# Kernel tuning notes

Hardware: AMD Instinct MI355X
Metric: run time of the kernel (lower is better)

The kernel has to match this reference:

```python
import jax, jax.numpy as jnp
import numpy as np
import math

B, Q, CQ = 2, 2048, 512
H, D = 8, 64  # no_heads, c_hidden

def setup_inputs() -> dict:
    key = jax.random.key(0)
    ks = jax.random.split(key, 8)
    s = 0.02
    return {
        "q_x": jax.random.normal(ks[0], (B, Q, CQ), jnp.float32),
        "kv_x": jax.random.normal(ks[1], (B, Q, CQ), jnp.float32),
        "bias": jax.random.normal(ks[2], (B, 1, Q, Q), jnp.float32),
        "w_qkv": jax.random.normal(ks[3], (3 * H * D, CQ), jnp.float32) * s,
        "w_o": jax.random.normal(ks[4], (CQ, H * D), jnp.float32) * s,
        "b_o": jnp.zeros((CQ,), jnp.float32),
        "w_g": jax.random.normal(ks[5], (H * D, CQ), jnp.float32) * s,
        "b_g": jnp.zeros((H * D,), jnp.float32),
    }

def reference(q_x, kv_x, bias, w_qkv, w_o, b_o, w_g, b_g):
    # Fused QKV projection from q_x (kv_x is unused by the original module's _prep_qkv)
    qkv = jnp.einsum('bqc,ec->bqe', q_x, w_qkv)  # [B,Q,3*H*D]
    q, k, v = jnp.split(qkv, 3, axis=-1)
    q = q.reshape(B, Q, H, D) / math.sqrt(D)
    k = k.reshape(B, Q, H, D)
    v = v.reshape(B, Q, H, D)
    # scores + additive pairwise bias, softmax over keys
    scores = jnp.einsum('bqhd,bkhd->bhqk', q, k) + bias  # [B,H,Q,K]
    attn = jax.nn.softmax(scores, axis=-1)
    o = jnp.einsum('bhqk,bkhd->bqhd', attn, v)  # [B,Q,H,D]
    # sigmoid gating
    g = jax.nn.sigmoid(jnp.einsum('bqc,ec->bqe', q_x, w_g) + b_g).reshape(B, Q, H, D)
    o = o * g
    # output projection
    o = o.reshape(B, Q, H * D)
    return jnp.einsum('bqe,ce->bqc', o, w_o) + b_o
```

## Files before the change

kernel.cpp:

```cpp
#include <hip/hip_runtime.h>
#include <math.h>

#define B_  2
#define Q_  2048
#define CQ_ 512
#define H_  8
#define D_  64
#define M_  (B_*Q_)

typedef __bf16 bf16;
typedef __bf16 bf16x4 __attribute__((ext_vector_type(4)));
typedef __bf16 bf16x8 __attribute__((ext_vector_type(8)));
typedef float  f32x4  __attribute__((ext_vector_type(4)));

__device__ __forceinline__ void gl_lds16(const bf16* g, bf16* l) {
    __builtin_amdgcn_global_load_lds(
        (const __attribute__((address_space(1))) unsigned int*)g,
        (__attribute__((address_space(3))) unsigned int*)l, 16, 0, 0);
}

#define S0 (4096*512)
#define S1 (1536*512)
#define S2 (512*512)
#define S3 (512*512)
__global__ __launch_bounds__(256)
void convert_kernel(const float* __restrict__ qx, const float* __restrict__ wqkv,
                    const float* __restrict__ wg, const float* __restrict__ wo,
                    bf16* __restrict__ qxb, bf16* __restrict__ wcat, bf16* __restrict__ wob)
{
    const long long t = (long long)blockIdx.x * 256 + threadIdx.x;
    const long long e = t * 8;
    const float* src; bf16* dst;
    if (e < S0)                { src = qx + e;                  dst = qxb + e; }
    else if (e < S0 + S1)      { src = wqkv + (e - S0);         dst = wcat + (e - S0); }
    else if (e < S0 + S1 + S2) { src = wg + (e - S0 - S1);      dst = wcat + S1 + (e - S0 - S1); }
    else                       { src = wo + (e - S0 - S1 - S2); dst = wob + (e - S0 - S1 - S2); }
    const float4 a = *(const float4*)(src);
    const float4 b = *(const float4*)(src + 4);
    bf16x8 v;
    v[0] = (bf16)a.x; v[1] = (bf16)a.y; v[2] = (bf16)a.z; v[3] = (bf16)a.w;
    v[4] = (bf16)b.x; v[5] = (bf16)b.y; v[6] = (bf16)b.z; v[7] = (bf16)b.w;
    *(bf16x8*)dst = v;
}

template<int BM, int BN, int EPI>
__global__ __launch_bounds__(256)
void gemm_bf16(const bf16* __restrict__ A, const bf16* __restrict__ W,
               const float* __restrict__ bvec, float* __restrict__ fout,
               bf16* __restrict__ qb, bf16* __restrict__ kb, bf16* __restrict__ vb,
               bf16* __restrict__ gb)
{
    constexpr int MI = BM / 32, NJ = BN / 32;
    __shared__ __align__(16) bf16 As[BM * 32];
    __shared__ __align__(16) bf16 Bs[BN * 32];

    const int t = threadIdx.x;
    const int w = t >> 6, lane = t & 63;
    const int l15 = lane & 15, quad = lane >> 4;
    const int wm = w & 1, wn = w >> 1;
    const int bm = blockIdx.x * BM;
    const int bn = blockIdx.y * BN;

    f32x4 acc[MI][NJ] = {};

    const int rr = t >> 2;
    const int cc = (t & 3) * 8;

    for (int k0 = 0; k0 < 512; k0 += 32) {
        #pragma unroll
        for (int i = 0; i < BM / 64; ++i)
            gl_lds16(A + (size_t)(bm + i * 64 + rr) * 512 + k0 + cc,
                     As + (i * 64 + w * 16) * 32);
        #pragma unroll
        for (int i = 0; i < BN / 64; ++i)
            gl_lds16(W + (size_t)(bn + i * 64 + rr) * 512 + k0 + cc,
                     Bs + (i * 64 + w * 16) * 32);
        __asm__ volatile("s_waitcnt vmcnt(0)" ::: "memory");
        __syncthreads();

        bf16x8 af[MI], bfr[NJ];
        #pragma unroll
        for (int i = 0; i < MI; ++i)
            af[i] = *(const bf16x8*)(As + (wm * (BM / 2) + i * 16 + l15) * 32 + quad * 8);
        #pragma unroll
        for (int j = 0; j < NJ; ++j)
            bfr[j] = *(const bf16x8*)(Bs + (wn * (BN / 2) + j * 16 + l15) * 32 + quad * 8);
        #pragma unroll
        for (int i = 0; i < MI; ++i)
            #pragma unroll
            for (int j = 0; j < NJ; ++j)
                acc[i][j] = __builtin_amdgcn_mfma_f32_16x16x32_bf16(af[i], bfr[j], acc[i][j], 0, 0, 0);
        __syncthreads();
    }

    #pragma unroll
    for (int i = 0; i < MI; ++i) {
        #pragma unroll
        for (int r = 0; r < 4; ++r) {
            const int m = bm + wm * (BM / 2) + i * 16 + quad * 4 + r;
            const int b = m >> 11, qq = m & 2047;
            #pragma unroll
            for (int j = 0; j < NJ; ++j) {
                const int n = bn + wn * (BN / 2) + j * 16 + l15;
                const float c = acc[i][j][r];
                if constexpr (EPI == 0) {
                    const int part = n >> 9;
                    const int h = (n >> 6) & 7, d = n & 63;
                    if (part == 0)
                        qb[(((size_t)(b * H_ + h)) * Q_ + qq) * D_ + d] = (bf16)(c * 0.125f);
                    else if (part == 1)
                        kb[(((size_t)(b * H_ + h)) * Q_ + qq) * D_ + d] = (bf16)c;
                    else if (part == 2)
                        vb[(((size_t)(b * H_ + h)) * D_ + d) * Q_ + qq] = (bf16)c;
                    else {
                        const int gcol = n & 511;
                        const float x = c + bvec[gcol];
                        gb[(size_t)m * 512 + gcol] = (bf16)(1.f / (1.f + __expf(-x)));
                    }
                } else {
                    fout[(size_t)m * 512 + n] = c + bvec[n];
                }
            }
        }
    }
}

__global__ __launch_bounds__(256)
void attn_kernel(const bf16* __restrict__ qb, const bf16* __restrict__ kb,
                 const bf16* __restrict__ vb, const float* __restrict__ bias,
                 const bf16* __restrict__ g, bf16* __restrict__ og)
{
    __shared__ __align__(16) bf16 Ks[2][64 * 72];
    __shared__ __align__(16) bf16 Vs[2][64 * 72];
    __shared__ __align__(16) bf16 Ps[4][16 * 72];

    const int tid  = threadIdx.x;
    const int wv   = tid >> 6, lane = tid & 63;
    const int l15  = lane & 15, quad = lane >> 4;
    const int bh   = blockIdx.x;
    const int b    = bh >> 3, h = bh & 7;
    const int q0   = blockIdx.y * 64;
    const int qrow = q0 + wv * 16 + l15;

    const bf16* qptr = qb + ((size_t)bh * Q_ + qrow) * D_;
    const bf16x8 bq0 = *(const bf16x8*)(qptr + quad * 8);
    const bf16x8 bq1 = *(const bf16x8*)(qptr + 32 + quad * 8);

    f32x4 acc[4] = {};
    float m_run = -INFINITY, l_run = 0.f;

    const bf16*  kbase = kb + (size_t)bh * Q_ * D_;
    const bf16*  vbase = vb + (size_t)bh * D_ * Q_;
    const float* brow  = bias + ((size_t)b * Q_ + qrow) * Q_;

    const int sr  = tid >> 3;
    const int sc8 = (tid & 7) * 8;

    float4 kreg0, kreg1, vreg0, vreg1;
    float4 bias_cur[4], bias_nxt[4];

    kreg0 = *(const float4*)(kbase + (size_t)sr * 64 + sc8);
    kreg1 = *(const float4*)(kbase + (size_t)(32 + sr) * 64 + sc8);
    vreg0 = *(const float4*)(vbase + (size_t)sr * Q_ + sc8);
    vreg1 = *(const float4*)(vbase + (size_t)(32 + sr) * Q_ + sc8);
    #pragma unroll
    for (int kt = 0; kt < 4; ++kt)
        bias_cur[kt] = *(const float4*)(brow + kt * 16 + quad * 4);
    *(float4*)(Ks[0] + sr * 72 + sc8) = kreg0;
    *(float4*)(Ks[0] + (32 + sr) * 72 + sc8) = kreg1;
    *(float4*)(Vs[0] + sr * 72 + sc8) = vreg0;
    *(float4*)(Vs[0] + (32 + sr) * 72 + sc8) = vreg1;
    __syncthreads();

    int cur = 0;
    for (int t = 0; t < 32; ++t) {
        if (t < 31) {
            const int k0n = (t + 1) * 64;
            kreg0 = *(const float4*)(kbase + ((size_t)k0n + sr) * 64 + sc8);
            kreg1 = *(const float4*)(kbase + ((size_t)k0n + 32 + sr) * 64 + sc8);
            vreg0 = *(const float4*)(vbase + (size_t)sr * Q_ + k0n + sc8);
            vreg1 = *(const float4*)(vbase + (size_t)(32 + sr) * Q_ + k0n + sc8);
            #pragma unroll
            for (int kt = 0; kt < 4; ++kt)
                bias_nxt[kt] = *(const float4*)(brow + k0n + kt * 16 + quad * 4);
        }

        const bf16* Kc = Ks[cur];
        const bf16* Vc = Vs[cur];

        float sc[4][4];
        #pragma unroll
        for (int kt = 0; kt < 4; ++kt) {
            f32x4 sacc = {0.f, 0.f, 0.f, 0.f};
            const bf16* kp = Kc + (kt * 16 + l15) * 72 + quad * 8;
            const bf16x8 ak0 = *(const bf16x8*)(kp);
            const bf16x8 ak1 = *(const bf16x8*)(kp + 32);
            sacc = __builtin_amdgcn_mfma_f32_16x16x32_bf16(ak0, bq0, sacc, 0, 0, 0);
            sacc = __builtin_amdgcn_mfma_f32_16x16x32_bf16(ak1, bq1, sacc, 0, 0, 0);
            sc[kt][0] = sacc[0] + bias_cur[kt].x;
            sc[kt][1] = sacc[1] + bias_cur[kt].y;
            sc[kt][2] = sacc[2] + bias_cur[kt].z;
            sc[kt][3] = sacc[3] + bias_cur[kt].w;
        }

        float tmax = -INFINITY;
        #pragma unroll
        for (int kt = 0; kt < 4; ++kt)
            tmax = fmaxf(tmax, fmaxf(fmaxf(sc[kt][0], sc[kt][1]),
                                     fmaxf(sc[kt][2], sc[kt][3])));
        tmax = fmaxf(tmax, __shfl_xor(tmax, 16, 64));
        tmax = fmaxf(tmax, __shfl_xor(tmax, 32, 64));

        const float mn = fmaxf(m_run, tmax);
        const float alpha = __expf(m_run - mn);
        m_run = mn;

        float rsum = 0.f;
        #pragma unroll
        for (int kt = 0; kt < 4; ++kt)
            #pragma unroll
            for (int r = 0; r < 4; ++r) {
                sc[kt][r] = __expf(sc[kt][r] - mn);
                rsum += sc[kt][r];
            }
        rsum += __shfl_xor(rsum, 16, 64);
        rsum += __shfl_xor(rsum, 32, 64);
        l_run = l_run * alpha + rsum;
        #pragma unroll
        for (int dt = 0; dt < 4; ++dt) acc[dt] *= alpha;

        bf16* pw = Ps[wv] + l15 * 72;
        #pragma unroll
        for (int kt = 0; kt < 4; ++kt) {
            bf16x4 p4;
            p4[0] = (bf16)sc[kt][0]; p4[1] = (bf16)sc[kt][1];
            p4[2] = (bf16)sc[kt][2]; p4[3] = (bf16)sc[kt][3];
            *(bf16x4*)(pw + kt * 16 + quad * 4) = p4;
        }
        __asm__ volatile("s_waitcnt lgkmcnt(0)" ::: "memory");

        #pragma unroll
        for (int kt2 = 0; kt2 < 2; ++kt2) {
            const bf16x8 bp = *(const bf16x8*)(pw + kt2 * 32 + quad * 8);
            #pragma unroll
            for (int dt = 0; dt < 4; ++dt) {
                const bf16x8 av = *(const bf16x8*)(Vc + (dt * 16 + l15) * 72 + kt2 * 32 + quad * 8);
                acc[dt] = __builtin_amdgcn_mfma_f32_16x16x32_bf16(av, bp, acc[dt], 0, 0, 0);
            }
        }

        if (t < 31) {
            *(float4*)(Ks[cur ^ 1] + sr * 72 + sc8) = kreg0;
            *(float4*)(Ks[cur ^ 1] + (32 + sr) * 72 + sc8) = kreg1;
            *(float4*)(Vs[cur ^ 1] + sr * 72 + sc8) = vreg0;
            *(float4*)(Vs[cur ^ 1] + (32 + sr) * 72 + sc8) = vreg1;
            #pragma unroll
            for (int kt = 0; kt < 4; ++kt) bias_cur[kt] = bias_nxt[kt];
        }
        __syncthreads();
        cur ^= 1;
    }

    const float inv = 1.f / l_run;
    const size_t obase = ((size_t)(b * Q_ + qrow)) * 512 + h * 64;
    #pragma unroll
    for (int dt = 0; dt < 4; ++dt) {
        const bf16x4 gv = *(const bf16x4*)(g + obase + dt * 16 + quad * 4);
        bf16x4 ov;
        #pragma unroll
        for (int r = 0; r < 4; ++r)
            ov[r] = (bf16)(acc[dt][r] * inv * (float)gv[r]);
        *(bf16x4*)(og + obase + dt * 16 + quad * 4) = ov;
    }
}

extern "C" void kernel_launch(void* const* d_in, const int* in_sizes, int n_in,
                              void* d_out, int out_size, void* d_ws, size_t ws_size,
                              hipStream_t stream)
{
    const float* q_x   = (const float*)d_in[0];
    const float* bias  = (const float*)d_in[2];
    const float* w_qkv = (const float*)d_in[3];
    const float* w_o   = (const float*)d_in[4];
    const float* b_o   = (const float*)d_in[5];
    const float* w_g   = (const float*)d_in[6];
    const float* b_g   = (const float*)d_in[7];
    float* out = (float*)d_out;

    char* ws = (char*)d_ws;
    bf16* qxb  = (bf16*)(ws);
    bf16* wcat = (bf16*)(ws + (4u  << 20));
    bf16* wob  = (bf16*)(ws + (6u  << 20));
    bf16* qb   = (bf16*)(ws + (8u  << 20));
    bf16* kb   = (bf16*)(ws + (12u << 20));
    bf16* vb   = (bf16*)(ws + (16u << 20));
    bf16* gb   = (bf16*)(ws + (20u << 20));
    bf16* ogb  = (bf16*)(ws + (24u << 20));

    convert_kernel<<<(S0 + S1 + S2 + S3) / (256 * 8), 256, 0, stream>>>(
        q_x, w_qkv, w_g, w_o, qxb, wcat, wob);
    gemm_bf16<128, 128, 0><<<dim3(32, 16), 256, 0, stream>>>(
        qxb, wcat, b_g, nullptr, qb, kb, vb, gb);
    attn_kernel<<<dim3(B_ * H_, Q_ / 64), 256, 0, stream>>>(qb, kb, vb, bias, gb, ogb);
    gemm_bf16<64, 128, 1><<<dim3(64, 4), 256, 0, stream>>>(
        ogb, wob, b_o, out, nullptr, nullptr, nullptr, nullptr);
}
```

Before: 180.8 us.

## Pre-swizzle K/V into MFMA fragment layout and load directly to registers

The QKV projection epilogue now writes K and V in a fragment-ordered layout, so each wave can load its MFMA operands straight from global memory into registers. This removes the LDS staging of K/V and the per-tile __syncthreads. Softmax switches to exp2, with log2(e) folded into the Q scale and the bias FMA, and blocks are remapped so both batches interleave. Each wave now redundantly fetches the full K/V tile from global/L2, which raises register pressure (launch_bounds 256,2) and puts more load on the cache.

```diff
diff --git a/kernel.cpp b/kernel.cpp
--- a/kernel.cpp
+++ b/kernel.cpp
@@ -7,6 +7,7 @@
 #define H_  8
 #define D_  64
 #define M_  (B_*Q_)
+#define L2E 1.44269504088896f
 
 typedef __bf16 bf16;
 typedef __bf16 bf16x4 __attribute__((ext_vector_type(4)));
@@ -102,45 +103,47 @@
             #pragma unroll
             for (int j = 0; j < NJ; ++j) {
                 const int n = bn + wn * (BN / 2) + j * 16 + l15;
-                const float c = acc[i][j][r];
+                const float cval = acc[i][j][r];
                 if constexpr (EPI == 0) {
                     const int part = n >> 9;
                     const int h = (n >> 6) & 7, d = n & 63;
-                    if (part == 0)
-                        qb[(((size_t)(b * H_ + h)) * Q_ + qq) * D_ + d] = (bf16)(c * 0.125f);
-                    else if (part == 1)
-                        kb[(((size_t)(b * H_ + h)) * Q_ + qq) * D_ + d] = (bf16)c;
-                    else if (part == 2)
-                        vb[(((size_t)(b * H_ + h)) * D_ + d) * Q_ + qq] = (bf16)c;
-                    else {
+                    const size_t bhbase = (size_t)(b * H_ + h) * (Q_ * D_);
+                    if (part == 0) {
+                        qb[bhbase + (size_t)qq * D_ + d] = (bf16)(cval * (0.125f * L2E));
+                    } else if (part == 1) {
+                        const int rg = qq >> 4, ll = qq & 15, ch = d >> 3, jj = d & 7;
+                        kb[bhbase + rg * 1024 + ch * 128 + ll * 8 + jj] = (bf16)cval;
+                    } else if (part == 2) {
+                        const int tile = qq >> 6, kc2 = (qq & 63) >> 3, jj = qq & 7;
+                        const int dt = d >> 4, dl = d & 15;
+                        vb[bhbase + tile * 4096 + dt * 1024 + kc2 * 128 + dl * 8 + jj] = (bf16)cval;
+                    } else {
                         const int gcol = n & 511;
-                        const float x = c + bvec[gcol];
+                        const float x = cval + bvec[gcol];
                         gb[(size_t)m * 512 + gcol] = (bf16)(1.f / (1.f + __expf(-x)));
                     }
                 } else {
-                    fout[(size_t)m * 512 + n] = c + bvec[n];
+                    fout[(size_t)m * 512 + n] = cval + bvec[n];
                 }
             }
         }
     }
 }
 
-__global__ __launch_bounds__(256)
-void attn_kernel(const bf16* __restrict__ qb, const bf16* __restrict__ kb,
-                 const bf16* __restrict__ vb, const float* __restrict__ bias,
+__global__ __launch_bounds__(256, 2)
+void attn_kernel(const bf16* __restrict__ qb, const bf16* __restrict__ kf,
+                 const bf16* __restrict__ vf, const float* __restrict__ bias,
                  const bf16* __restrict__ g, bf16* __restrict__ og)
 {
-    __shared__ __align__(16) bf16 Ks[2][64 * 72];
-    __shared__ __align__(16) bf16 Vs[2][64 * 72];
     __shared__ __align__(16) bf16 Ps[4][16 * 72];
 
     const int tid  = threadIdx.x;
     const int wv   = tid >> 6, lane = tid & 63;
     const int l15  = lane & 15, quad = lane >> 4;
-    const int bh   = blockIdx.x;
+    const int x    = blockIdx.x;
+    const int bh   = ((x & 1) << 3) | (x >> 1);
     const int b    = bh >> 3, h = bh & 7;
-    const int q0   = blockIdx.y * 64;
-    const int qrow = q0 + wv * 16 + l15;
+    const int qrow = blockIdx.y * 64 + wv * 16 + l15;
 
     const bf16* qptr = qb + ((size_t)bh * Q_ + qrow) * D_;
     const bf16x8 bq0 = *(const bf16x8*)(qptr + quad * 8);
@@ -149,58 +152,49 @@
     f32x4 acc[4] = {};
     float m_run = -INFINITY, l_run = 0.f;
 
-    const bf16*  kbase = kb + (size_t)bh * Q_ * D_;
-    const bf16*  vbase = vb + (size_t)bh * D_ * Q_;
-    const float* brow  = bias + ((size_t)b * Q_ + qrow) * Q_;
-
-    const int sr  = tid >> 3;
-    const int sc8 = (tid & 7) * 8;
-
-    float4 kreg0, kreg1, vreg0, vreg1;
-    float4 bias_cur[4], bias_nxt[4];
-
-    kreg0 = *(const float4*)(kbase + (size_t)sr * 64 + sc8);
-    kreg1 = *(const float4*)(kbase + (size_t)(32 + sr) * 64 + sc8);
-    vreg0 = *(const float4*)(vbase + (size_t)sr * Q_ + sc8);
-    vreg1 = *(const float4*)(vbase + (size_t)(32 + sr) * Q_ + sc8);
+    const bf16*  kfb  = kf + (size_t)bh * (Q_ * D_);
+    const bf16*  vfb  = vf + (size_t)bh * (Q_ * D_);
+    const float* brow = bias + ((size_t)b * Q_ + qrow) * Q_;
+
+    bf16x8 kc[8], vc[8], kn[8], vn[8];
+    float4 bc[4], bn4[4];
+
     #pragma unroll
-    for (int kt = 0; kt < 4; ++kt)
-        bias_cur[kt] = *(const float4*)(brow + kt * 16 + quad * 4);
-    *(float4*)(Ks[0] + sr * 72 + sc8) = kreg0;
-    *(float4*)(Ks[0] + (32 + sr) * 72 + sc8) = kreg1;
-    *(float4*)(Vs[0] + sr * 72 + sc8) = vreg0;
-    *(float4*)(Vs[0] + (32 + sr) * 72 + sc8) = vreg1;
-    __syncthreads();
-
-    int cur = 0;
+    for (int kt = 0; kt < 4; ++kt) {
+        kc[kt * 2]     = *(const bf16x8*)(kfb + (kt * 8 + quad) * 128 + l15 * 8);
+        kc[kt * 2 + 1] = *(const bf16x8*)(kfb + (kt * 8 + quad + 4) * 128 + l15 * 8);
+        vc[kt * 2]     = *(const bf16x8*)(vfb + (kt * 8 + quad) * 128 + l15 * 8);
+        vc[kt * 2 + 1] = *(const bf16x8*)(vfb + (kt * 8 + quad + 4) * 128 + l15 * 8);
+        bc[kt] = *(const float4*)(brow + kt * 16 + quad * 4);
+    }
+
+    bf16* pw = Ps[wv] + l15 * 72;
+
+    #pragma unroll 2
     for (int t = 0; t < 32; ++t) {
         if (t < 31) {
-            const int k0n = (t + 1) * 64;
-            kreg0 = *(const float4*)(kbase + ((size_t)k0n + sr) * 64 + sc8);
-            kreg1 = *(const float4*)(kbase + ((size_t)k0n + 32 + sr) * 64 + sc8);
-            vreg0 = *(const float4*)(vbase + (size_t)sr * Q_ + k0n + sc8);
-            vreg1 = *(const float4*)(vbase + (size_t)(32 + sr) * Q_ + k0n + sc8);
-            #pragma unroll
-            for (int kt = 0; kt < 4; ++kt)
-                bias_nxt[kt] = *(const float4*)(brow + k0n + kt * 16 + quad * 4);
-        }
-
-        const bf16* Kc = Ks[cur];
-        const bf16* Vc = Vs[cur];
+            const int off = (t + 1) * 4096;
+            const int boff = (t + 1) * 64;
+            #pragma unroll
+            for (int kt = 0; kt < 4; ++kt) {
+                kn[kt * 2]     = *(const bf16x8*)(kfb + off + (kt * 8 + quad) * 128 + l15 * 8);
+                kn[kt * 2 + 1] = *(const bf16x8*)(kfb + off + (kt * 8 + quad + 4) * 128 + l15 * 8);
+                vn[kt * 2]     = *(const bf16x8*)(vfb + off + (kt * 8 + quad) * 128 + l15 * 8);
+                vn[kt * 2 + 1] = *(const bf16x8*)(vfb + off + (kt * 8 + quad + 4) * 128 + l15 * 8);
+                bn4[kt] = *(const float4*)(brow + boff + kt * 16 + quad * 4);
+            }
+        }
 
         float sc[4][4];
         #pragma unroll
         for (int kt = 0; kt < 4; ++kt) {
             f32x4 sacc = {0.f, 0.f, 0.f, 0.f};
-            const bf16* kp = Kc + (kt * 16 + l15) * 72 + quad * 8;
-            const bf16x8 ak0 = *(const bf16x8*)(kp);
-            const bf16x8 ak1 = *(const bf16x8*)(kp + 32);
-            sacc = __builtin_amdgcn_mfma_f32_16x16x32_bf16(ak0, bq0, sacc, 0, 0, 0);
-            sacc = __builtin_amdgcn_mfma_f32_16x16x32_bf16(ak1, bq1, sacc, 0, 0, 0);
-            sc[kt][0] = sacc[0] + bias_cur[kt].x;
-            sc[kt][1] = sacc[1] + bias_cur[kt].y;
-            sc[kt][2] = sacc[2] + bias_cur[kt].z;
-            sc[kt][3] = sacc[3] + bias_cur[kt].w;
+            sacc = __builtin_amdgcn_mfma_f32_16x16x32_bf16(kc[kt * 2],     bq0, sacc, 0, 0, 0);
+            sacc = __builtin_amdgcn_mfma_f32_16x16x32_bf16(kc[kt * 2 + 1], bq1, sacc, 0, 0, 0);
+            sc[kt][0] = fmaf(bc[kt].x, L2E, sacc[0]);
+            sc[kt][1] = fmaf(bc[kt].y, L2E, sacc[1]);
+            sc[kt][2] = fmaf(bc[kt].z, L2E, sacc[2]);
+            sc[kt][3] = fmaf(bc[kt].w, L2E, sacc[3]);
         }
 
         float tmax = -INFINITY;
@@ -212,7 +206,7 @@
         tmax = fmaxf(tmax, __shfl_xor(tmax, 32, 64));
 
         const float mn = fmaxf(m_run, tmax);
-        const float alpha = __expf(m_run - mn);
+        const float alpha = __builtin_amdgcn_exp2f(m_run - mn);
         m_run = mn;
 
         float rsum = 0.f;
@@ -220,7 +214,7 @@
         for (int kt = 0; kt < 4; ++kt)
             #pragma unroll
             for (int r = 0; r < 4; ++r) {
-                sc[kt][r] = __expf(sc[kt][r] - mn);
+                sc[kt][r] = __builtin_amdgcn_exp2f(sc[kt][r] - mn);
                 rsum += sc[kt][r];
             }
         rsum += __shfl_xor(rsum, 16, 64);
@@ -229,7 +223,6 @@
         #pragma unroll
         for (int dt = 0; dt < 4; ++dt) acc[dt] *= alpha;
 
-        bf16* pw = Ps[wv] + l15 * 72;
         #pragma unroll
         for (int kt = 0; kt < 4; ++kt) {
             bf16x4 p4;
@@ -243,22 +236,16 @@
         for (int kt2 = 0; kt2 < 2; ++kt2) {
             const bf16x8 bp = *(const bf16x8*)(pw + kt2 * 32 + quad * 8);
             #pragma unroll
-            for (int dt = 0; dt < 4; ++dt) {
-                const bf16x8 av = *(const bf16x8*)(Vc + (dt * 16 + l15) * 72 + kt2 * 32 + quad * 8);
-                acc[dt] = __builtin_amdgcn_mfma_f32_16x16x32_bf16(av, bp, acc[dt], 0, 0, 0);
-            }
+            for (int dt = 0; dt < 4; ++dt)
+                acc[dt] = __builtin_amdgcn_mfma_f32_16x16x32_bf16(vc[dt * 2 + kt2], bp, acc[dt], 0, 0, 0);
         }
 
         if (t < 31) {
-            *(float4*)(Ks[cur ^ 1] + sr * 72 + sc8) = kreg0;
-            *(float4*)(Ks[cur ^ 1] + (32 + sr) * 72 + sc8) = kreg1;
-            *(float4*)(Vs[cur ^ 1] + sr * 72 + sc8) = vreg0;
-            *(float4*)(Vs[cur ^ 1] + (32 + sr) * 72 + sc8) = vreg1;
-            #pragma unroll
-            for (int kt = 0; kt < 4; ++kt) bias_cur[kt] = bias_nxt[kt];
-        }
-        __syncthreads();
-        cur ^= 1;
+            #pragma unroll
+            for (int i = 0; i < 8; ++i) { kc[i] = kn[i]; vc[i] = vn[i]; }
+            #pragma unroll
+            for (int kt = 0; kt < 4; ++kt) bc[kt] = bn4[kt];
+        }
     }
 
     const float inv = 1.f / l_run;
```

After: 205.3 us. 1.14x slower.
